# Optimization experiments

Measured on AMD Instinct MI355X. Metric: run time of the kernel, lower is better.

The kernel has to match this reference:

```python
import jax, jax.numpy as jnp
import numpy as np

B, F, D = 16384, 32, 64   # batch, n_continuous_features, input_dim
H = 2 * D                  # hidden = 2*input_dim per the d_hidden spec


def setup_inputs() -> dict:
    key = jax.random.key(0)
    ks = jax.random.split(key, 6)
    s1 = 1.0 / np.sqrt(D).astype(np.float32)
    s2 = 1.0 / np.sqrt(H).astype(np.float32)
    return {
        "X": jax.random.normal(ks[0], (B, F), jnp.float32),
        "r_": jax.random.normal(ks[1], (B, F, D), jnp.float32),
        # stacked per-feature weights (one tiny MLP per continuous column)
        "W1": jax.random.normal(ks[2], (F, D, H), jnp.float32) * s1,
        "b1": jax.random.normal(ks[3], (F, H), jnp.float32) * s1,
        "W2": jax.random.normal(ks[4], (F, H, 1), jnp.float32) * s2,
        "b2": jax.random.normal(ks[5], (F, 1), jnp.float32) * s2,
    }


def reference(X, r_, W1, b1, W2, b2):
    # Per-feature 2-layer MLP (Linear->relu->Linear->relu), batched over the
    # feature axis instead of the original Python loop over ModuleDict.
    h = jax.nn.relu(jnp.einsum('bfd,fdh->bfh', r_, W1) + b1)   # [B,F,H]
    y = jax.nn.relu(jnp.einsum('bfh,fho->bfo', h, W2) + b2)    # [B,F,1]
    x = X[..., None]                                           # [B,F,1] raw scalar per column
    # Original returns list of (x_col, mlp_out) pairs; we pack them as [B,F,2]
    # with [...,0]=x and [...,1]=mlp output (same values, dense layout).
    return jnp.concatenate([x, y], axis=-1)
```

## Files before the change

kernel.cpp:

```cpp
#include <hip/hip_runtime.h>
#include <hip/hip_bf16.h>
#include <stdint.h>

#define B_SZ 16384
#define F_SZ 32
#define D_SZ 64
#define H_SZ 128

typedef __attribute__((ext_vector_type(8))) short  short8;
typedef __attribute__((ext_vector_type(4))) float  float4v;
typedef __attribute__((ext_vector_type(4))) unsigned int uint4v;

__device__ __forceinline__ unsigned int pkbf(float lo, float hi) {
  unsigned int ulo = __builtin_bit_cast(unsigned int, lo) + 0x8000u;
  unsigned int uhi = __builtin_bit_cast(unsigned int, hi) + 0x8000u;
  return __builtin_amdgcn_perm(uhi, ulo, 0x07060302u);
}

__global__ __launch_bounds__(256) void ContMlp_prep(
    const float* __restrict__ W1, const float* __restrict__ b1,
    const float* __restrict__ W2, unsigned short* __restrict__ w1t,
    unsigned int* __restrict__ bw) {
  const int f = blockIdx.x;
  const int t = threadIdx.x;
  __shared__ float lds[D_SZ][H_SZ + 1];
  const float* w1f = W1 + (size_t)f * (D_SZ * H_SZ);
#pragma unroll
  for (int i = 0; i < 32; ++i) {
    int e = t + 256 * i;
    lds[e >> 7][e & 127] = w1f[e];
  }
  __syncthreads();
  unsigned short* o = w1t + (size_t)f * (H_SZ * D_SZ);
#pragma unroll
  for (int i = 0; i < 32; ++i) {
    int e = t + 256 * i;
    int h = e >> 6, d = e & 63;
    unsigned int u = __builtin_bit_cast(unsigned int, lds[d][h]) + 0x8000u;
    o[e] = (unsigned short)(u >> 16);
  }
  if (t < H_SZ) {
    unsigned int ub = __builtin_bit_cast(unsigned int, b1[f * H_SZ + t]) + 0x8000u;
    unsigned int uw = __builtin_bit_cast(unsigned int, W2[f * H_SZ + t]) + 0x8000u;
    bw[f * H_SZ + t] = (ub & 0xFFFF0000u) | (uw >> 16);
  }
}

__global__ __launch_bounds__(256, 3) void ContMlp_main(
    const float* __restrict__ X, const float* __restrict__ r_,
    const unsigned short* __restrict__ w1t, const unsigned int* __restrict__ bw,
    const float* __restrict__ b2, float* __restrict__ out) {
  const int f    = blockIdx.x & 31;
  const int tile = blockIdx.x >> 5;
  const int w    = threadIdx.x >> 6;
  const int l    = threadIdx.x & 63;
  const int col  = l & 15;
  const int quad = l >> 4;

  const unsigned short* w1f = w1t + (size_t)f * (H_SZ * D_SZ);
  short8 afrag[8][2];
#pragma unroll
  for (int t = 0; t < 8; ++t)
#pragma unroll
    for (int ks = 0; ks < 2; ++ks) {
      const uint4v* p = (const uint4v*)(w1f + (col + 16 * t) * D_SZ + ks * 32 + quad * 8);
      afrag[t][ks] = __builtin_bit_cast(short8, *p);
    }
  uint4v bwreg[8];
#pragma unroll
  for (int t = 0; t < 8; ++t)
    bwreg[t] = *(const uint4v*)(bw + f * H_SZ + 16 * t + quad * 4);
  const float b2f = b2[f];

  const int b_wave = tile * 256 + w * 64;
#pragma unroll
  for (int s = 0; s < 4; ++s) {
    const int b0  = b_wave + s * 16;
    const int row = b0 + col;
    const float* rp = r_ + (size_t)row * (F_SZ * D_SZ) + f * D_SZ + quad * 8;
    float4v r0 = *(const float4v*)(rp);
    float4v r1 = *(const float4v*)(rp + 4);
    float4v r2 = *(const float4v*)(rp + 32);
    float4v r3 = *(const float4v*)(rp + 36);

    unsigned int p0 = pkbf(r0.x, r0.y), p1 = pkbf(r0.z, r0.w);
    unsigned int p2 = pkbf(r1.x, r1.y), p3 = pkbf(r1.z, r1.w);
    unsigned int p4 = pkbf(r2.x, r2.y), p5 = pkbf(r2.z, r2.w);
    unsigned int p6 = pkbf(r3.x, r3.y), p7 = pkbf(r3.z, r3.w);
    uint4v bq0 = {p0, p1, p2, p3};
    uint4v bq1 = {p4, p5, p6, p7};
    short8 bfrag0 = __builtin_bit_cast(short8, bq0);
    short8 bfrag1 = __builtin_bit_cast(short8, bq1);

    float4v acc[8];
#pragma unroll
    for (int t = 0; t < 8; ++t) acc[t] = {0.f, 0.f, 0.f, 0.f};
#pragma unroll
    for (int t = 0; t < 8; ++t) {
      acc[t] = __builtin_amdgcn_mfma_f32_16x16x32_bf16(afrag[t][0], bfrag0, acc[t], 0, 0, 0);
      acc[t] = __builtin_amdgcn_mfma_f32_16x16x32_bf16(afrag[t][1], bfrag1, acc[t], 0, 0, 0);
    }

    float ysum = 0.f;
#pragma unroll
    for (int t = 0; t < 8; ++t)
#pragma unroll
      for (int r = 0; r < 4; ++r) {
        unsigned int u = bwreg[t][r];
        float b1v = __builtin_bit_cast(float, u & 0xFFFF0000u);
        float w2v = __builtin_bit_cast(float, u << 16);
        float hv  = fmaxf(acc[t][r] + b1v, 0.f);
        ysum = fmaf(hv, w2v, ysum);
      }
    ysum += __shfl_xor(ysum, 16, 64);
    ysum += __shfl_xor(ysum, 32, 64);
    float y = fmaxf(ysum + b2f, 0.f);

    if (quad == 0) {
      float xv = X[row * F_SZ + f];
      float2 o2 = make_float2(xv, y);
      *(float2*)(out + (size_t)row * (F_SZ * 2) + f * 2) = o2;
    }
  }
}

extern "C" void kernel_launch(void* const* d_in, const int* in_sizes, int n_in,
                              void* d_out, int out_size, void* d_ws, size_t ws_size,
                              hipStream_t stream) {
  const float* X  = (const float*)d_in[0];
  const float* r_ = (const float*)d_in[1];
  const float* W1 = (const float*)d_in[2];
  const float* b1 = (const float*)d_in[3];
  const float* W2 = (const float*)d_in[4];
  const float* b2 = (const float*)d_in[5];
  float* out = (float*)d_out;

  unsigned short* w1t = (unsigned short*)d_ws;
  unsigned int*   bw  = (unsigned int*)((char*)d_ws + (size_t)F_SZ * H_SZ * D_SZ * 2);

  ContMlp_prep<<<F_SZ, 256, 0, stream>>>(W1, b1, W2, w1t, bw);
  ContMlp_main<<<(B_SZ / 256) * F_SZ, 256, 0, stream>>>(X, r_, w1t, bw, b2, out);
}
```

Baseline: 237.4 us.

## Stage W1 in LDS, double-buffer r_ loads, split output into combine kernel

```diff
diff --git a/kernel.cpp b/kernel.cpp
--- a/kernel.cpp
+++ b/kernel.cpp
@@ -6,6 +6,7 @@
 #define F_SZ 32
 #define D_SZ 64
 #define H_SZ 128
+#define RSTRIDE 72
 
 typedef __attribute__((ext_vector_type(8))) short  short8;
 typedef __attribute__((ext_vector_type(4))) float  float4v;
@@ -21,35 +22,76 @@
     const float* __restrict__ W1, const float* __restrict__ b1,
     const float* __restrict__ W2, unsigned short* __restrict__ w1t,
     unsigned int* __restrict__ bw) {
-  const int f = blockIdx.x;
-  const int t = threadIdx.x;
-  __shared__ float lds[D_SZ][H_SZ + 1];
+  const int f  = blockIdx.x >> 2;
+  const int hq = blockIdx.x & 3;
+  const int h0 = hq * 32;
+  const int t  = threadIdx.x;
+  __shared__ float lds[D_SZ][33];
   const float* w1f = W1 + (size_t)f * (D_SZ * H_SZ);
 #pragma unroll
-  for (int i = 0; i < 32; ++i) {
-    int e = t + 256 * i;
-    lds[e >> 7][e & 127] = w1f[e];
+  for (int i = 0; i < 8; ++i) {
+    int idx = t + 256 * i;
+    int d = idx >> 5, hh = idx & 31;
+    lds[d][hh] = w1f[d * H_SZ + h0 + hh];
   }
   __syncthreads();
   unsigned short* o = w1t + (size_t)f * (H_SZ * D_SZ);
 #pragma unroll
-  for (int i = 0; i < 32; ++i) {
-    int e = t + 256 * i;
-    int h = e >> 6, d = e & 63;
-    unsigned int u = __builtin_bit_cast(unsigned int, lds[d][h]) + 0x8000u;
-    o[e] = (unsigned short)(u >> 16);
-  }
-  if (t < H_SZ) {
+  for (int i = 0; i < 8; ++i) {
+    int idx = t + 256 * i;
+    int hh = idx >> 6, d = idx & 63;
+    unsigned int u = __builtin_bit_cast(unsigned int, lds[d][hh]) + 0x8000u;
+    o[(h0 + hh) * D_SZ + d] = (unsigned short)(u >> 16);
+  }
+  if (hq == 0 && t < H_SZ) {
     unsigned int ub = __builtin_bit_cast(unsigned int, b1[f * H_SZ + t]) + 0x8000u;
     unsigned int uw = __builtin_bit_cast(unsigned int, W2[f * H_SZ + t]) + 0x8000u;
     bw[f * H_SZ + t] = (ub & 0xFFFF0000u) | (uw >> 16);
   }
 }
 
-__global__ __launch_bounds__(256, 3) void ContMlp_main(
-    const float* __restrict__ X, const float* __restrict__ r_,
+__device__ __forceinline__ void compute_sub(
+    float4v c0, float4v c1, float4v c2, float4v c3,
+    const unsigned short* w1l, const unsigned int* bwl,
+    float b2f, int col, int quad, float* store_ptr) {
+  unsigned int p0 = pkbf(c0.x, c0.y), p1 = pkbf(c0.z, c0.w);
+  unsigned int p2 = pkbf(c1.x, c1.y), p3 = pkbf(c1.z, c1.w);
+  unsigned int p4 = pkbf(c2.x, c2.y), p5 = pkbf(c2.z, c2.w);
+  unsigned int p6 = pkbf(c3.x, c3.y), p7 = pkbf(c3.z, c3.w);
+  uint4v bq0 = {p0, p1, p2, p3};
+  uint4v bq1 = {p4, p5, p6, p7};
+  short8 bf0 = __builtin_bit_cast(short8, bq0);
+  short8 bf1 = __builtin_bit_cast(short8, bq1);
+
+  float ysum = 0.f;
+#pragma unroll
+  for (int t = 0; t < 8; ++t) {
+    const unsigned short* wrow = w1l + (col + 16 * t) * RSTRIDE + quad * 8;
+    short8 a0 = *(const short8*)(wrow);
+    short8 a1 = *(const short8*)(wrow + 32);
+    float4v acc = {0.f, 0.f, 0.f, 0.f};
+    acc = __builtin_amdgcn_mfma_f32_16x16x32_bf16(a0, bf0, acc, 0, 0, 0);
+    acc = __builtin_amdgcn_mfma_f32_16x16x32_bf16(a1, bf1, acc, 0, 0, 0);
+    uint4v bwv = *(const uint4v*)(bwl + 16 * t + quad * 4);
+#pragma unroll
+    for (int r = 0; r < 4; ++r) {
+      unsigned int u = bwv[r];
+      float b1v = __builtin_bit_cast(float, u & 0xFFFF0000u);
+      float w2v = __builtin_bit_cast(float, u << 16);
+      ysum = fmaf(fmaxf(acc[r] + b1v, 0.f), w2v, ysum);
+    }
+  }
+  ysum += __shfl_xor(ysum, 16, 64);
+  ysum += __shfl_xor(ysum, 32, 64);
+  float y = fmaxf(ysum + b2f, 0.f);
+  if (quad == 0) *store_ptr = y;
+}
+
+__global__ void ContMlp_main(
+    const float* __restrict__ r_,
     const unsigned short* __restrict__ w1t, const unsigned int* __restrict__ bw,
-    const float* __restrict__ b2, float* __restrict__ out) {
+    const float* __restrict__ b2, float* __restrict__ ydst,
+    int y_fmul, int y_rmul, int y_cadd) {
   const int f    = blockIdx.x & 31;
   const int tile = blockIdx.x >> 5;
   const int w    = threadIdx.x >> 6;
@@ -57,71 +99,76 @@
   const int col  = l & 15;
   const int quad = l >> 4;
 
-  const unsigned short* w1f = w1t + (size_t)f * (H_SZ * D_SZ);
-  short8 afrag[8][2];
-#pragma unroll
-  for (int t = 0; t < 8; ++t)
-#pragma unroll
-    for (int ks = 0; ks < 2; ++ks) {
-      const uint4v* p = (const uint4v*)(w1f + (col + 16 * t) * D_SZ + ks * 32 + quad * 8);
-      afrag[t][ks] = __builtin_bit_cast(short8, *p);
+  __shared__ unsigned short w1l[H_SZ * RSTRIDE];
+  __shared__ unsigned int   bwl[H_SZ];
+
+  {
+    const uint4v* src = (const uint4v*)(w1t + (size_t)f * (H_SZ * D_SZ));
+#pragma unroll
+    for (int i = 0; i < 4; ++i) {
+      int ci = threadIdx.x + 256 * i;
+      int h = ci >> 3, dc = ci & 7;
+      *(uint4v*)(w1l + h * RSTRIDE + dc * 8) = src[ci];
     }
-  uint4v bwreg[8];
-#pragma unroll
-  for (int t = 0; t < 8; ++t)
-    bwreg[t] = *(const uint4v*)(bw + f * H_SZ + 16 * t + quad * 4);
+    if (threadIdx.x < H_SZ) bwl[threadIdx.x] = bw[f * H_SZ + threadIdx.x];
+  }
+  __syncthreads();
   const float b2f = b2[f];
 
-  const int b_wave = tile * 256 + w * 64;
-#pragma unroll
-  for (int s = 0; s < 4; ++s) {
-    const int b0  = b_wave + s * 16;
-    const int row = b0 + col;
-    const float* rp = r_ + (size_t)row * (F_SZ * D_SZ) + f * D_SZ + quad * 8;
-    float4v r0 = *(const float4v*)(rp);
-    float4v r1 = *(const float4v*)(rp + 4);
-    float4v r2 = *(const float4v*)(rp + 32);
-    float4v r3 = *(const float4v*)(rp + 36);
-
-    unsigned int p0 = pkbf(r0.x, r0.y), p1 = pkbf(r0.z, r0.w);
-    unsigned int p2 = pkbf(r1.x, r1.y), p3 = pkbf(r1.z, r1.w);
-    unsigned int p4 = pkbf(r2.x, r2.y), p5 = pkbf(r2.z, r2.w);
-    unsigned int p6 = pkbf(r3.x, r3.y), p7 = pkbf(r3.z, r3.w);
-    uint4v bq0 = {p0, p1, p2, p3};
-    uint4v bq1 = {p4, p5, p6, p7};
-    short8 bfrag0 = __builtin_bit_cast(short8, bq0);
-    short8 bfrag1 = __builtin_bit_cast(short8, bq1);
-
-    float4v acc[8];
-#pragma unroll
-    for (int t = 0; t < 8; ++t) acc[t] = {0.f, 0.f, 0.f, 0.f};
-#pragma unroll
-    for (int t = 0; t < 8; ++t) {
-      acc[t] = __builtin_amdgcn_mfma_f32_16x16x32_bf16(afrag[t][0], bfrag0, acc[t], 0, 0, 0);
-      acc[t] = __builtin_amdgcn_mfma_f32_16x16x32_bf16(afrag[t][1], bfrag1, acc[t], 0, 0, 0);
-    }
-
-    float ysum = 0.f;
-#pragma unroll
-    for (int t = 0; t < 8; ++t)
-#pragma unroll
-      for (int r = 0; r < 4; ++r) {
-        unsigned int u = bwreg[t][r];
-        float b1v = __builtin_bit_cast(float, u & 0xFFFF0000u);
-        float w2v = __builtin_bit_cast(float, u << 16);
-        float hv  = fmaxf(acc[t][r] + b1v, 0.f);
-        ysum = fmaf(hv, w2v, ysum);
-      }
-    ysum += __shfl_xor(ysum, 16, 64);
-    ysum += __shfl_xor(ysum, 32, 64);
-    float y = fmaxf(ysum + b2f, 0.f);
-
-    if (quad == 0) {
-      float xv = X[row * F_SZ + f];
-      float2 o2 = make_float2(xv, y);
-      *(float2*)(out + (size_t)row * (F_SZ * 2) + f * 2) = o2;
-    }
-  }
+  const int row_w0 = tile * 256 + w * 64;
+  const float* rbase = r_ + (size_t)(row_w0 + col) * (F_SZ * D_SZ)
+                          + f * D_SZ + quad * 8;
+
+#define LOADSUB(S, N)                                                   \
+  do {                                                                  \
+    const float* p_ = rbase + (size_t)(S) * 16 * (F_SZ * D_SZ);         \
+    N##0 = *(const float4v*)(p_);      N##1 = *(const float4v*)(p_ + 4);\
+    N##2 = *(const float4v*)(p_ + 32); N##3 = *(const float4v*)(p_ + 36);\
+  } while (0)
+
+#define YPTR(S) (ydst + (size_t)f * y_fmul                               \
+                     + (size_t)(row_w0 + (S)*16 + col) * y_rmul + y_cadd)
+
+  float4v A0, A1, A2, A3, Bb0, Bb1, Bb2, Bb3;
+  LOADSUB(0, A);
+  LOADSUB(1, Bb);
+  compute_sub(A0, A1, A2, A3, w1l, bwl, b2f, col, quad, YPTR(0));
+  LOADSUB(2, A);
+  compute_sub(Bb0, Bb1, Bb2, Bb3, w1l, bwl, b2f, col, quad, YPTR(1));
+  LOADSUB(3, Bb);
+  compute_sub(A0, A1, A2, A3, w1l, bwl, b2f, col, quad, YPTR(2));
+  compute_sub(Bb0, Bb1, Bb2, Bb3, w1l, bwl, b2f, col, quad, YPTR(3));
+#undef LOADSUB
+#undef YPTR
+}
+
+__global__ __launch_bounds__(256) void ContMlp_combine(
+    const float* __restrict__ X, const float* __restrict__ yws,
+    float* __restrict__ out) {
+  __shared__ float yl[F_SZ][33];
+  const int r0 = blockIdx.x * 32;
+  const int t = threadIdx.x;
+#pragma unroll
+  for (int i = 0; i < 4; ++i) {
+    int idx = t + 256 * i;
+    int f = idx >> 5, r = idx & 31;
+    yl[f][r] = yws[(size_t)f * B_SZ + r0 + r];
+  }
+  __syncthreads();
+#pragma unroll
+  for (int i = 0; i < 4; ++i) {
+    int idx = t + 256 * i;
+    int r = idx >> 5, f = idx & 31;
+    float2 o2 = make_float2(X[(size_t)(r0 + r) * F_SZ + f], yl[f][r]);
+    *(float2*)(out + (size_t)(r0 + r) * (2 * F_SZ) + 2 * f) = o2;
+  }
+}
+
+__global__ __launch_bounds__(256) void ContMlp_xwrite(
+    const float* __restrict__ X, float* __restrict__ out) {
+  int idx = blockIdx.x * 256 + threadIdx.x;
+  int r = idx >> 5, f = idx & 31;
+  out[(size_t)r * (2 * F_SZ) + 2 * f] = X[idx];
 }
 
 extern "C" void kernel_launch(void* const* d_in, const int* in_sizes, int n_in,
@@ -135,9 +182,26 @@
   const float* b2 = (const float*)d_in[5];
   float* out = (float*)d_out;
 
+  const size_t w1t_bytes = (size_t)F_SZ * H_SZ * D_SZ * 2;
+  const size_t bw_off    = w1t_bytes;
+  const size_t bw_bytes  = (size_t)F_SZ * H_SZ * 4;
+  const size_t y_off     = bw_off + bw_bytes;
+  const size_t y_bytes   = (size_t)B_SZ * F_SZ * 4;
+
   unsigned short* w1t = (unsigned short*)d_ws;
-  unsigned int*   bw  = (unsigned int*)((char*)d_ws + (size_t)F_SZ * H_SZ * D_SZ * 2);
-
-  ContMlp_prep<<<F_SZ, 256, 0, stream>>>(W1, b1, W2, w1t, bw);
-  ContMlp_main<<<(B_SZ / 256) * F_SZ, 256, 0, stream>>>(X, r_, w1t, bw, b2, out);
-}
+  unsigned int*   bw  = (unsigned int*)((char*)d_ws + bw_off);
+
+  ContMlp_prep<<<F_SZ * 4, 256, 0, stream>>>(W1, b1, W2, w1t, bw);
+
+  const bool pathA = ws_size >= y_off + y_bytes;
+  if (pathA) {
+    float* yws = (float*)((char*)d_ws + y_off);
+    ContMlp_main<<<64 * F_SZ, 256, 0, stream>>>(r_, w1t, bw, b2, yws,
+                                                B_SZ, 1, 0);
+    ContMlp_combine<<<B_SZ / 32, 256, 0, stream>>>(X, yws, out);
+  } else {
+    ContMlp_main<<<64 * F_SZ, 256, 0, stream>>>(r_, w1t, bw, b2, out,
+                                                2, 2 * F_SZ, 1);
+    ContMlp_xwrite<<<(B_SZ * F_SZ) / 256, 256, 0, stream>>>(X, out);
+  }
+}
```

After: 259.0 us. 1.09x slower.
